# Kernel tuning notes

Hardware: AMD Instinct MI355X
Metric: run time of the kernel (lower is better)

## Reference

```python
import jax, jax.numpy as jnp
import numpy as np

N, E, G, H = 50000, 800000, 64, 4
IN_DIM, HID, OUT = 768, 256, 128
EPS = 1e-5
SLOPE = 0.2


def _glorot(k, shape):
    lim = np.sqrt(6.0 / (shape[0] + shape[1])).astype(np.float32)
    return jax.random.uniform(k, shape, jnp.float32, -lim, lim)


def setup_inputs() -> dict:
    key = jax.random.key(0)
    ks = jax.random.split(key, 24)
    inp = {
        'x': jax.random.normal(ks[0], (N, IN_DIM), jnp.float32),
        'edge_index': jax.random.randint(ks[1], (2, E), 0, N, jnp.int32),
        'batch': jnp.sort(jax.random.randint(ks[2], (N,), 0, G, jnp.int32)),
    }
    dims = [(IN_DIM, HID), (HID, HID), (HID, OUT)]
    for i, (di, do) in enumerate(dims, start=1):
        c = do // H
        inp[f'W{i}'] = _glorot(ks[3 * i], (di, do))
        inp[f'asrc{i}'] = _glorot(ks[3 * i + 1], (H, c))
        inp[f'adst{i}'] = _glorot(ks[3 * i + 2], (H, c))
        inp[f'b{i}'] = jnp.zeros((do,), jnp.float32)
        inp[f'g{i}'] = jnp.ones((do,), jnp.float32)
        inp[f'be{i}'] = jnp.zeros((do,), jnp.float32)
    return inp


def gat_conv(x, src, dst, W, asrc, adst, b):
    # PyG GATConv, concat=True, negative_slope=0.2, self-loops pre-appended.
    n = x.shape[0]
    HC = W.shape[1]
    C = HC // H
    h = (x @ W).reshape(n, H, C)                 # [N,H,C]
    e_src = (h * asrc).sum(-1)                   # [N,H]
    e_dst = (h * adst).sum(-1)                   # [N,H]
    e = jax.nn.leaky_relu(e_src[src] + e_dst[dst], SLOPE)  # [E',H]
    m = jax.ops.segment_max(e, dst, num_segments=n)
    p = jnp.exp(e - m[dst])
    denom = jax.ops.segment_sum(p, dst, num_segments=n)
    alpha = p / denom[dst]                       # segment softmax over in-edges
    out = jax.ops.segment_sum(alpha[:, :, None] * h[src], dst, num_segments=n)
    return out.reshape(n, HC) + b


def layer_norm(x, g, b):
    mu = x.mean(-1, keepdims=True)
    var = x.var(-1, keepdims=True)
    return g * (x - mu) * jax.lax.rsqrt(var + EPS) + b


def reference(x, edge_index, batch, W1, asrc1, adst1, b1, g1, be1,
              W2, asrc2, adst2, b2, g2, be2, W3, asrc3, adst3, b3, g3, be3):
    n = x.shape[0]
    loops = jnp.arange(n, dtype=edge_index.dtype)
    src = jnp.concatenate([edge_index[0], loops])
    dst = jnp.concatenate([edge_index[1], loops])
    h = gat_conv(x, src, dst, W1, asrc1, adst1, b1)
    h = layer_norm(jax.nn.elu(h), g1, be1)
    h = gat_conv(h, src, dst, W2, asrc2, adst2, b2)
    h = layer_norm(jax.nn.elu(h), g2, be2)
    h = gat_conv(h, src, dst, W3, asrc3, adst3, b3)
    node_emb = layer_norm(h, g3, be3)
    s = jax.ops.segment_sum(node_emb, batch, num_segments=G)
    cnt = jax.ops.segment_sum(jnp.ones((n, 1), node_emb.dtype), batch, num_segments=G)
    graph_emb = s / jnp.maximum(cnt, 1.0)
    return (node_emb, graph_emb)
```

## Files before the change

kernel.cpp:

```cpp
#include <hip/hip_runtime.h>
#include <math.h>

__device__ __forceinline__ float lrelu(float v) { return v > 0.f ? v : 0.2f * v; }
__device__ __forceinline__ float bf2f(ushort u) {
    return __uint_as_float(((unsigned int)u) << 16);
}
__device__ __forceinline__ ushort f2bf(float f) {
    unsigned int x = __float_as_uint(f);
    return (ushort)((x + 0x7fffu + ((x >> 16) & 1u)) >> 16);
}
__device__ __forceinline__ float wave_allred_sum(float v) {
#pragma unroll
    for (int off = 1; off < 64; off <<= 1) v += __shfl_xor(v, off, 64);
    return v;
}

typedef short bf16x8 __attribute__((ext_vector_type(8)));
typedef float f32x4 __attribute__((ext_vector_type(4)));

__global__ void hist_kernel(const int* __restrict__ dstrow, int* __restrict__ cnt,
                            int Etot, int E) {
    int i = blockIdx.x * blockDim.x + threadIdx.x;
    if (i >= Etot) return;
    int d = (i < E) ? dstrow[i] : (i - E);
    atomicAdd(&cnt[d], 1);
}

__global__ __launch_bounds__(256) void scan1_kernel(const int* __restrict__ cnt,
                                                    int* __restrict__ out,
                                                    int* __restrict__ btot, int n) {
    __shared__ int s[256];
    int i = blockIdx.x * 256 + threadIdx.x;
    int v = (i < n) ? cnt[i] : 0;
    s[threadIdx.x] = v;
    __syncthreads();
    for (int off = 1; off < 256; off <<= 1) {
        int t = (threadIdx.x >= off) ? s[threadIdx.x - off] : 0;
        __syncthreads();
        s[threadIdx.x] += t;
        __syncthreads();
    }
    if (i < n) out[i] = s[threadIdx.x];
    if (threadIdx.x == 255) btot[blockIdx.x] = s[255];
}
__global__ __launch_bounds__(1024) void scan2_kernel(int* __restrict__ btot, int nb) {
    __shared__ int s[1024];
    int tid = threadIdx.x;
    int v = (tid < nb) ? btot[tid] : 0;
    s[tid] = v;
    __syncthreads();
    for (int off = 1; off < 1024; off <<= 1) {
        int t = (tid >= off) ? s[tid - off] : 0;
        __syncthreads();
        s[tid] += t;
        __syncthreads();
    }
    if (tid < nb) btot[tid] = s[tid] - v;
}
__global__ void scan3_kernel(const int* __restrict__ scanned, const int* __restrict__ btot,
                             int* __restrict__ rowptr, int n) {
    int i = blockIdx.x * 256 + threadIdx.x;
    if (i < n) rowptr[i + 1] = scanned[i] + btot[i >> 8];
    if (i == 0) rowptr[0] = 0;
}

__global__ void fill_kernel(const int* __restrict__ srcrow, const int* __restrict__ dstrow,
                            const int* __restrict__ rowptr, int* __restrict__ pos,
                            int* __restrict__ srcs, int Etot, int E) {
    int i = blockIdx.x * blockDim.x + threadIdx.x;
    if (i >= Etot) return;
    int d = (i < E) ? dstrow[i] : (i - E);
    int s = (i < E) ? srcrow[i] : (i - E);
    int p = atomicAdd(&pos[d], 1);
    srcs[rowptr[d] + p] = s;
}

template <typename TA>
__global__ __launch_bounds__(256) void gemm_mfma(const TA* __restrict__ A,
                                                 const float* __restrict__ B,
                                                 ushort* __restrict__ C, int M, int K, int N) {
    __shared__ ushort As[128][40];
    __shared__ ushort Bs[128][40];
    int tid = threadIdx.x;
    int wave = tid >> 6, lane = tid & 63;
    int m0 = blockIdx.y * 128, n0 = blockIdx.x * 128;

    f32x4 acc[2][8] = {};

    int arow = tid >> 1;
    int ak = (tid & 1) * 16;
    int bk = tid >> 3;
    int bn = (tid & 7) * 16;

    int quad = lane >> 4;
    int mrow = lane & 15;

    for (int kt = 0; kt < K; kt += 32) {
        if (m0 + arow < M) {
            if constexpr (sizeof(TA) == 4) {
                const float* p = (const float*)A + (size_t)(m0 + arow) * K + kt + ak;
#pragma unroll
                for (int q = 0; q < 4; q++) {
                    float4 v = *(const float4*)(p + q * 4);
                    ushort* d = &As[arow][ak + q * 4];
                    d[0] = f2bf(v.x); d[1] = f2bf(v.y); d[2] = f2bf(v.z); d[3] = f2bf(v.w);
                }
            } else {
                const ushort* p = (const ushort*)A + (size_t)(m0 + arow) * K + kt + ak;
                *(uint4*)&As[arow][ak] = *(const uint4*)p;
                *(uint4*)&As[arow][ak + 8] = *(const uint4*)(p + 8);
            }
        } else {
#pragma unroll
            for (int q = 0; q < 16; q++) As[arow][ak + q] = 0;
        }
        {
            const float* p = B + (size_t)(kt + bk) * N + n0 + bn;
#pragma unroll
            for (int q = 0; q < 4; q++) {
                float4 v = *(const float4*)(p + q * 4);
                Bs[bn + q * 4 + 0][bk] = f2bf(v.x);
                Bs[bn + q * 4 + 1][bk] = f2bf(v.y);
                Bs[bn + q * 4 + 2][bk] = f2bf(v.z);
                Bs[bn + q * 4 + 3][bk] = f2bf(v.w);
            }
        }
        __syncthreads();
        bf16x8 afrag[2], bfrag[8];
#pragma unroll
        for (int r = 0; r < 2; r++)
            afrag[r] = *(const bf16x8*)&As[wave * 32 + r * 16 + mrow][quad * 8];
#pragma unroll
        for (int c = 0; c < 8; c++)
            bfrag[c] = *(const bf16x8*)&Bs[c * 16 + mrow][quad * 8];
#pragma unroll
        for (int r = 0; r < 2; r++)
#pragma unroll
            for (int c = 0; c < 8; c++)
                acc[r][c] = __builtin_amdgcn_mfma_f32_16x16x32_bf16(afrag[r], bfrag[c],
                                                                    acc[r][c], 0, 0, 0);
        __syncthreads();
    }
    int col = lane & 15;
#pragma unroll
    for (int r = 0; r < 2; r++) {
#pragma unroll
        for (int c = 0; c < 8; c++) {
#pragma unroll
            for (int reg = 0; reg < 4; reg++) {
                int gm = m0 + wave * 32 + r * 16 + quad * 4 + reg;
                int gn = n0 + c * 16 + col;
                if (gm < M) C[(size_t)gm * N + gn] = f2bf(acc[r][c][reg]);
            }
        }
    }
}

template <int VPL>
__global__ __launch_bounds__(256) void attn_wave(const ushort* __restrict__ H,
                                                 const float* __restrict__ asrc,
                                                 const float* __restrict__ adst,
                                                 float* __restrict__ es, float* __restrict__ ed,
                                                 int N) {
    constexpr int HC = VPL * 64;
    int lane = threadIdx.x & 63;
    int node = (blockIdx.x * blockDim.x + threadIdx.x) >> 6;
    if (node >= N) return;
    const ushort* hp = H + (size_t)node * HC + lane * VPL;
    float esum = 0.f, dsum = 0.f;
#pragma unroll
    for (int j = 0; j < VPL; j++) {
        float h = bf2f(hp[j]);
        int ch = lane * VPL + j;
        esum += h * asrc[ch];
        dsum += h * adst[ch];
    }
#pragma unroll
    for (int off = 1; off < 16; off <<= 1) {
        esum += __shfl_xor(esum, off, 64);
        dsum += __shfl_xor(dsum, off, 64);
    }
    if ((lane & 15) == 0) {
        int hh = lane >> 4;
        es[node * 4 + hh] = esum;
        ed[node * 4 + hh] = dsum;
    }
}

template <int VPL>
__global__ __launch_bounds__(256) void agg_gather(
    const ushort* __restrict__ H, const float* __restrict__ es, const float* __restrict__ ed,
    const int* __restrict__ rowptr, const int* __restrict__ srcs,
    const float* __restrict__ bias, const float* __restrict__ gamma,
    const float* __restrict__ beta, ushort* __restrict__ XoutB, float* __restrict__ XoutF,
    int N, int applyElu) {
    constexpr int HC = VPL * 64;
    int lane = threadIdx.x & 63;
    int node = (blockIdx.x * blockDim.x + threadIdx.x) >> 6;
    if (node >= N) return;
    int base = rowptr[node];
    int deg = rowptr[node + 1] - base;
    float4 ed4 = *(const float4*)&ed[node * 4];

    float4 sm = make_float4(0.f, 0.f, 0.f, 0.f);
    for (int i = lane; i < deg; i += 64) {
        int s = srcs[base + i];
        float4 e4 = *(const float4*)&es[(size_t)s * 4];
        sm.x += __expf(lrelu(e4.x + ed4.x));
        sm.y += __expf(lrelu(e4.y + ed4.y));
        sm.z += __expf(lrelu(e4.z + ed4.z));
        sm.w += __expf(lrelu(e4.w + ed4.w));
    }
    sm.x = wave_allred_sum(sm.x); sm.y = wave_allred_sum(sm.y);
    sm.z = wave_allred_sum(sm.z); sm.w = wave_allred_sum(sm.w);

    int hh = lane >> 4;
    float rd_h = 1.f / ((hh == 0) ? sm.x : (hh == 1) ? sm.y : (hh == 2) ? sm.z : sm.w);
    float edh = (hh == 0) ? ed4.x : (hh == 1) ? ed4.y : (hh == 2) ? ed4.z : ed4.w;

    float acc[VPL];
#pragma unroll
    for (int j = 0; j < VPL; j++) acc[j] = 0.f;
    const ushort* Hl = H + lane * VPL;

    int i = 0;
    for (; i + 2 <= deg; i += 2) {
        int s0 = srcs[base + i];
        int s1 = srcs[base + i + 1];
        float e0 = es[(size_t)s0 * 4 + hh];
        float e1 = es[(size_t)s1 * 4 + hh];
        const ushort* hp0 = Hl + (size_t)s0 * HC;
        const ushort* hp1 = Hl + (size_t)s1 * HC;
        float a0 = __expf(lrelu(e0 + edh)) * rd_h;
        float a1 = __expf(lrelu(e1 + edh)) * rd_h;
        if constexpr (VPL == 4) {
            ushort4 h0 = *(const ushort4*)hp0;
            ushort4 h1 = *(const ushort4*)hp1;
            acc[0] += a0 * bf2f(h0.x) + a1 * bf2f(h1.x);
            acc[1] += a0 * bf2f(h0.y) + a1 * bf2f(h1.y);
            acc[2] += a0 * bf2f(h0.z) + a1 * bf2f(h1.z);
            acc[3] += a0 * bf2f(h0.w) + a1 * bf2f(h1.w);
        } else {
            ushort2 h0 = *(const ushort2*)hp0;
            ushort2 h1 = *(const ushort2*)hp1;
            acc[0] += a0 * bf2f(h0.x) + a1 * bf2f(h1.x);
            acc[1] += a0 * bf2f(h0.y) + a1 * bf2f(h1.y);
        }
    }
    for (; i < deg; i++) {
        int s = srcs[base + i];
        float a = __expf(lrelu(es[(size_t)s * 4 + hh] + edh)) * rd_h;
        const ushort* hp = Hl + (size_t)s * HC;
        if constexpr (VPL == 4) {
            ushort4 hv = *(const ushort4*)hp;
            acc[0] += a * bf2f(hv.x); acc[1] += a * bf2f(hv.y);
            acc[2] += a * bf2f(hv.z); acc[3] += a * bf2f(hv.w);
        } else {
            ushort2 hv = *(const ushort2*)hp;
            acc[0] += a * bf2f(hv.x); acc[1] += a * bf2f(hv.y);
        }
    }

    float v[VPL];
    float s1 = 0.f, s2 = 0.f;
#pragma unroll
    for (int j = 0; j < VPL; j++) {
        int ch = lane * VPL + j;
        float t = acc[j] + bias[ch];
        if (applyElu) t = (t > 0.f) ? t : (__expf(t) - 1.f);
        v[j] = t;
        s1 += t;
        s2 += t * t;
    }
    s1 = wave_allred_sum(s1);
    s2 = wave_allred_sum(s2);
    float mu = s1 / (float)HC;
    float var = s2 / (float)HC - mu * mu;
    float rs = rsqrtf(var + 1e-5f);
#pragma unroll
    for (int j = 0; j < VPL; j++) {
        int ch = lane * VPL + j;
        float o = gamma[ch] * (v[j] - mu) * rs + beta[ch];
        if (XoutF) XoutF[(size_t)node * HC + ch] = o;
        else XoutB[(size_t)node * HC + ch] = f2bf(o);
    }
}

__global__ __launch_bounds__(128) void gsum_kernel(const float* __restrict__ node_emb,
                                                   const int* __restrict__ batch,
                                                   float* __restrict__ gsum,
                                                   int* __restrict__ gcnt, int N) {
    int start = blockIdx.x * 256;
    if (start >= N) return;
    int end = min(start + 256, N);
    int ch = threadIdx.x;
    float acc = 0.f;
    int runlen = 0;
    int curg = batch[start];
    for (int n = start; n < end; n++) {
        int g = batch[n];
        if (g != curg) {
            atomicAdd(&gsum[curg * 128 + ch], acc);
            if (ch == 0) atomicAdd(&gcnt[curg], runlen);
            acc = 0.f; runlen = 0; curg = g;
        }
        acc += node_emb[(size_t)n * 128 + ch];
        runlen++;
    }
    atomicAdd(&gsum[curg * 128 + ch], acc);
    if (ch == 0) atomicAdd(&gcnt[curg], runlen);
}

__global__ void gfinal_kernel(const float* __restrict__ gsum, const int* __restrict__ gcnt,
                              float* __restrict__ out, int Gn) {
    int i = blockIdx.x * blockDim.x + threadIdx.x;
    if (i >= Gn * 128) return;
    int g = i >> 7;
    out[i] = gsum[i] / fmaxf((float)gcnt[g], 1.f);
}

extern "C" void kernel_launch(void* const* d_in, const int* in_sizes, int n_in, void* d_out,
                              int out_size, void* d_ws, size_t ws_size, hipStream_t stream) {
    const float* x = (const float*)d_in[0];
    const int* ei = (const int*)d_in[1];
    const int* batch = (const int*)d_in[2];
    const float* W1 = (const float*)d_in[3];
    const float* as1 = (const float*)d_in[4];
    const float* ad1 = (const float*)d_in[5];
    const float* b1 = (const float*)d_in[6];
    const float* g1 = (const float*)d_in[7];
    const float* be1 = (const float*)d_in[8];
    const float* W2 = (const float*)d_in[9];
    const float* as2 = (const float*)d_in[10];
    const float* ad2 = (const float*)d_in[11];
    const float* b2 = (const float*)d_in[12];
    const float* g2 = (const float*)d_in[13];
    const float* be2 = (const float*)d_in[14];
    const float* W3 = (const float*)d_in[15];
    const float* as3 = (const float*)d_in[16];
    const float* ad3 = (const float*)d_in[17];
    const float* b3 = (const float*)d_in[18];
    const float* g3 = (const float*)d_in[19];
    const float* be3 = (const float*)d_in[20];

    int N = in_sizes[2];
    int E = in_sizes[1] / 2;
    int Etot = E + N;

    char* w = (char*)d_ws;
    size_t off = 0;
    auto alloc = [&](size_t bytes) -> void* {
        void* p = w + off;
        off += (bytes + 255) & ~(size_t)255;
        return p;
    };
    int* cnt = (int*)alloc((size_t)N * 4);
    int* pos = (int*)alloc((size_t)N * 4);
    float* gsum = (float*)alloc(64 * 128 * 4);
    int* gcnt = (int*)alloc(64 * 4);
    size_t zbytes = off;
    int* scantmp = (int*)alloc((size_t)N * 4);
    int* btot = (int*)alloc(1024 * 4);
    int* rowptr = (int*)alloc((size_t)(N + 1) * 4);
    int* srcs = (int*)alloc((size_t)Etot * 4);
    float* es = (float*)alloc((size_t)N * 16);
    float* ed = (float*)alloc((size_t)N * 16);
    ushort* Hb = (ushort*)alloc((size_t)N * 256 * 2);
    ushort* Xb = (ushort*)alloc((size_t)N * 256 * 2);

    hipMemsetAsync(d_ws, 0, zbytes, stream);

    const int* srcrow = ei;
    const int* dstrow = ei + E;

    int eb = (Etot + 255) / 256;
    int nb = (N + 255) / 256;
    hist_kernel<<<eb, 256, 0, stream>>>(dstrow, cnt, Etot, E);
    scan1_kernel<<<nb, 256, 0, stream>>>(cnt, scantmp, btot, N);
    scan2_kernel<<<1, 1024, 0, stream>>>(btot, nb);
    scan3_kernel<<<nb, 256, 0, stream>>>(scantmp, btot, rowptr, N);
    fill_kernel<<<eb, 256, 0, stream>>>(srcrow, dstrow, rowptr, pos, srcs, Etot, E);

    int mT = (N + 127) / 128;
    int nodeWaveBlocks = (N + 3) / 4;

    float* out_node = (float*)d_out;
    float* out_graph = (float*)d_out + (size_t)N * 128;

    gemm_mfma<float><<<dim3(2, mT), 256, 0, stream>>>(x, W1, Hb, N, 768, 256);
    attn_wave<4><<<nodeWaveBlocks, 256, 0, stream>>>(Hb, as1, ad1, es, ed, N);
    agg_gather<4><<<nodeWaveBlocks, 256, 0, stream>>>(Hb, es, ed, rowptr, srcs, b1, g1, be1,
                                                      Xb, nullptr, N, 1);
    gemm_mfma<ushort><<<dim3(2, mT), 256, 0, stream>>>(Xb, W2, Hb, N, 256, 256);
    attn_wave<4><<<nodeWaveBlocks, 256, 0, stream>>>(Hb, as2, ad2, es, ed, N);
    agg_gather<4><<<nodeWaveBlocks, 256, 0, stream>>>(Hb, es, ed, rowptr, srcs, b2, g2, be2,
                                                      Xb, nullptr, N, 1);
    gemm_mfma<ushort><<<dim3(1, mT), 256, 0, stream>>>(Xb, W3, Hb, N, 256, 128);
    attn_wave<2><<<nodeWaveBlocks, 256, 0, stream>>>(Hb, as3, ad3, es, ed, N);
    agg_gather<2><<<nodeWaveBlocks, 256, 0, stream>>>(Hb, es, ed, rowptr, srcs, b3, g3, be3,
                                                      nullptr, out_node, N, 0);
    gsum_kernel<<<(N + 255) / 256, 128, 0, stream>>>(out_node, batch, gsum, gcnt, N);
    gfinal_kernel<<<(64 * 128 + 255) / 256, 256, 0, stream>>>(gsum, gcnt, out_graph, 64);
}
```

Measured before the change: 820.7 us.

## Rewrite GEMM with async global-to-LDS double buffering and pretransposed bf16 weights

Weights are pre-transposed and converted to bf16 once per call by a new transpose kernel. The GEMM now stages A and B tiles straight into LDS with global_load_lds, double-buffered so the next K-slice loads while MFMAs run. It also uses XOR-swizzled LDS layouts to avoid bank conflicts and remaps workgroups across XCDs. The fp32 A tile is converted to bf16 at fragment-read time, which doubles LDS use for layer 1 and adds three small launches.

```diff
diff --git a/kernel.cpp b/kernel.cpp
--- a/kernel.cpp
+++ b/kernel.cpp
@@ -17,6 +17,12 @@
 
 typedef short bf16x8 __attribute__((ext_vector_type(8)));
 typedef float f32x4 __attribute__((ext_vector_type(4)));
+
+typedef const __attribute__((address_space(1))) void* gas_ptr;
+typedef __attribute__((address_space(3))) void* las_ptr;
+__device__ __forceinline__ void gload_lds16(const void* g, void* l) {
+    __builtin_amdgcn_global_load_lds((gas_ptr)g, (las_ptr)l, 16, 0, 0);
+}
 
 __global__ void hist_kernel(const int* __restrict__ dstrow, int* __restrict__ cnt,
                             int Etot, int E) {
@@ -75,64 +81,115 @@
     srcs[rowptr[d] + p] = s;
 }
 
+__global__ __launch_bounds__(256) void wconv_kernel(const float* __restrict__ W,
+                                                    ushort* __restrict__ Wt, int K, int N) {
+    __shared__ float t[32][33];
+    int k0 = blockIdx.x * 32, n0 = blockIdx.y * 32;
+    int tx = threadIdx.x & 31, ty = threadIdx.x >> 5;
+#pragma unroll
+    for (int i = 0; i < 32; i += 8)
+        t[ty + i][tx] = W[(size_t)(k0 + ty + i) * N + n0 + tx];
+    __syncthreads();
+#pragma unroll
+    for (int i = 0; i < 32; i += 8)
+        Wt[(size_t)(n0 + ty + i) * K + k0 + tx] = f2bf(t[tx][ty + i]);
+}
+
 template <typename TA>
-__global__ __launch_bounds__(256) void gemm_mfma(const TA* __restrict__ A,
-                                                 const float* __restrict__ B,
-                                                 ushort* __restrict__ C, int M, int K, int N) {
-    __shared__ ushort As[128][40];
-    __shared__ ushort Bs[128][40];
+__global__ __launch_bounds__(256) void gemm_mfma2(const TA* __restrict__ A,
+                                                  const ushort* __restrict__ Wt,
+                                                  ushort* __restrict__ C,
+                                                  int M, int K, int N) {
+    constexpr bool F32A = (sizeof(TA) == 4);
+    constexpr int ASZ = F32A ? 16384 : 8192;
+    __shared__ __align__(16) unsigned char smem[2 * ASZ + 16384];
+
     int tid = threadIdx.x;
-    int wave = tid >> 6, lane = tid & 63;
-    int m0 = blockIdx.y * 128, n0 = blockIdx.x * 128;
+    int wv = tid >> 6, lane = tid & 63;
+    int quad = lane >> 4, mrow = lane & 15;
+
+    int nwg = gridDim.x * gridDim.y;
+    int id = blockIdx.y * gridDim.x + blockIdx.x;
+    int q8 = nwg >> 3, r8 = nwg & 7;
+    int xcd = id & 7, loc = id >> 3;
+    int wgid = (xcd < r8 ? xcd * (q8 + 1) : r8 * (q8 + 1) + (xcd - r8) * q8) + loc;
+    int n0 = (wgid % gridDim.x) * 128;
+    int m0 = (wgid / gridDim.x) * 128;
 
     f32x4 acc[2][8] = {};
 
-    int arow = tid >> 1;
-    int ak = (tid & 1) * 16;
-    int bk = tid >> 3;
-    int bn = (tid & 7) * 16;
-
-    int quad = lane >> 4;
-    int mrow = lane & 15;
-
-    for (int kt = 0; kt < K; kt += 32) {
-        if (m0 + arow < M) {
-            if constexpr (sizeof(TA) == 4) {
-                const float* p = (const float*)A + (size_t)(m0 + arow) * K + kt + ak;
-#pragma unroll
-                for (int q = 0; q < 4; q++) {
-                    float4 v = *(const float4*)(p + q * 4);
-                    ushort* d = &As[arow][ak + q * 4];
-                    d[0] = f2bf(v.x); d[1] = f2bf(v.y); d[2] = f2bf(v.z); d[3] = f2bf(v.w);
-                }
-            } else {
-                const ushort* p = (const ushort*)A + (size_t)(m0 + arow) * K + kt + ak;
-                *(uint4*)&As[arow][ak] = *(const uint4*)p;
-                *(uint4*)&As[arow][ak + 8] = *(const uint4*)(p + 8);
+    auto stageA = [&](int kt, int buf) {
+        unsigned char* lb = smem + buf * ASZ;
+        if constexpr (F32A) {
+#pragma unroll
+            for (int q = 0; q < 4; q++) {
+                int row = q * 32 + (tid >> 3);
+                int gch = (tid & 7) ^ (row & 7);
+                int rc = min(m0 + row, M - 1);
+                gload_lds16((const float*)A + (size_t)rc * K + kt + gch * 4,
+                            lb + q * 4096 + tid * 16);
             }
         } else {
 #pragma unroll
-            for (int q = 0; q < 16; q++) As[arow][ak + q] = 0;
-        }
-        {
-            const float* p = B + (size_t)(kt + bk) * N + n0 + bn;
-#pragma unroll
-            for (int q = 0; q < 4; q++) {
-                float4 v = *(const float4*)(p + q * 4);
-                Bs[bn + q * 4 + 0][bk] = f2bf(v.x);
-                Bs[bn + q * 4 + 1][bk] = f2bf(v.y);
-                Bs[bn + q * 4 + 2][bk] = f2bf(v.z);
-                Bs[bn + q * 4 + 3][bk] = f2bf(v.w);
+            for (int q = 0; q < 2; q++) {
+                int row = q * 64 + (tid >> 2);
+                int gch = (tid & 3) ^ ((row & 3) ^ ((row >> 2) & 1));
+                int rc = min(m0 + row, M - 1);
+                gload_lds16((const ushort*)A + (size_t)rc * K + kt + gch * 8,
+                            lb + q * 4096 + tid * 16);
             }
         }
-        __syncthreads();
+    };
+    auto stageB = [&](int kt, int buf) {
+        unsigned char* lb = smem + 2 * ASZ + buf * 8192;
+#pragma unroll
+        for (int q = 0; q < 2; q++) {
+            int row = q * 64 + (tid >> 2);
+            int gch = (tid & 3) ^ ((row & 3) ^ ((row >> 2) & 1));
+            gload_lds16(Wt + (size_t)(n0 + row) * K + kt + gch * 8,
+                        lb + q * 4096 + tid * 16);
+        }
+    };
+
+    int nsteps = K >> 5;
+    stageA(0, 0);
+    stageB(0, 0);
+    __syncthreads();
+
+    for (int s = 0; s < nsteps; s++) {
+        int kt = s << 5;
+        if (s + 1 < nsteps) {
+            stageA(kt + 32, (s + 1) & 1);
+            stageB(kt + 32, (s + 1) & 1);
+        }
+        const unsigned char* la = smem + (s & 1) * ASZ;
+        const unsigned char* lbB = smem + 2 * ASZ + (s & 1) * 8192;
+
         bf16x8 afrag[2], bfrag[8];
 #pragma unroll
-        for (int r = 0; r < 2; r++)
-            afrag[r] = *(const bf16x8*)&As[wave * 32 + r * 16 + mrow][quad * 8];
-#pragma unroll
-        for (int c = 0; c < 8; c++)
-            bfrag[c] = *(const bf16x8*)&Bs[c * 16 + mrow][quad * 8];
+        for (int r = 0; r < 2; r++) {
+            int row = wv * 32 + r * 16 + mrow;
+            if constexpr (F32A) {
+                int f = row & 7;
+                float4 x0 = *(const float4*)(la + row * 128 + ((quad * 2 + 0) ^ f) * 16);
+                float4 x1 = *(const float4*)(la + row * 128 + ((quad * 2 + 1) ^ f) * 16);
+                union { bf16x8 v; ushort u[8]; } t;
+                t.u[0] = f2bf(x0.x); t.u[1] = f2bf(x0.y);
+                t.u[2] = f2bf(x0.z); t.u[3] = f2bf(x0.w);
+                t.u[4] = f2bf(x1.x); t.u[5] = f2bf(x1.y);
+                t.u[6] = f2bf(x1.z); t.u[7] = f2bf(x1.w);
+                afrag[r] = t.v;
+            } else {
+                int f = (row & 3) ^ ((row >> 2) & 1);
+                afrag[r] = *(const bf16x8*)(la + row * 64 + (quad ^ f) * 16);
+            }
+        }
+#pragma unroll
+        for (int c = 0; c < 8; c++) {
+            int row = c * 16 + mrow;
+            int f = (row & 3) ^ ((row >> 2) & 1);
+            bfrag[c] = *(const bf16x8*)(lbB + row * 64 + (quad ^ f) * 16);
+        }
 #pragma unroll
         for (int r = 0; r < 2; r++)
 #pragma unroll
@@ -141,6 +198,7 @@
                                                                     acc[r][c], 0, 0, 0);
         __syncthreads();
     }
+
     int col = lane & 15;
 #pragma unroll
     for (int r = 0; r < 2; r++) {
@@ -148,7 +206,7 @@
         for (int c = 0; c < 8; c++) {
 #pragma unroll
             for (int reg = 0; reg < 4; reg++) {
-                int gm = m0 + wave * 32 + r * 16 + quad * 4 + reg;
+                int gm = m0 + wv * 32 + r * 16 + quad * 4 + reg;
                 int gn = n0 + c * 16 + col;
                 if (gm < M) C[(size_t)gm * N + gn] = f2bf(acc[r][c][reg]);
             }
@@ -367,11 +425,18 @@
     float* ed = (float*)alloc((size_t)N * 16);
     ushort* Hb = (ushort*)alloc((size_t)N * 256 * 2);
     ushort* Xb = (ushort*)alloc((size_t)N * 256 * 2);
+    ushort* wt1 = (ushort*)alloc((size_t)768 * 256 * 2);
+    ushort* wt2 = (ushort*)alloc((size_t)256 * 256 * 2);
+    ushort* wt3 = (ushort*)alloc((size_t)256 * 128 * 2);
 
     hipMemsetAsync(d_ws, 0, zbytes, stream);
 
     const int* srcrow = ei;
     const int* dstrow = ei + E;
+
+    wconv_kernel<<<dim3(768 / 32, 256 / 32), 256, 0, stream>>>(W1, wt1, 768, 256);
+    wconv_kernel<<<dim3(256 / 32, 256 / 32), 256, 0, stream>>>(W2, wt2, 256, 256);
+    wconv_kernel<<<dim3(256 / 32, 128 / 32), 256, 0, stream>>>(W3, wt3, 256, 128);
 
     int eb = (Etot + 255) / 256;
     int nb = (N + 255) / 256;
@@ -387,15 +452,15 @@
     float* out_node = (float*)d_out;
     float* out_graph = (float*)d_out + (size_t)N * 128;
 
-    gemm_mfma<float><<<dim3(2, mT), 256, 0, stream>>>(x, W1, Hb, N, 768, 256);
+    gemm_mfma2<float><<<dim3(2, mT), 256, 0, stream>>>(x, wt1, Hb, N, 768, 256);
     attn_wave<4><<<nodeWaveBlocks, 256, 0, stream>>>(Hb, as1, ad1, es, ed, N);
     agg_gather<4><<<nodeWaveBlocks, 256, 0, stream>>>(Hb, es, ed, rowptr, srcs, b1, g1, be1,
                                                       Xb, nullptr, N, 1);
-    gemm_mfma<ushort><<<dim3(2, mT), 256, 0, stream>>>(Xb, W2, Hb, N, 256, 256);
+    gemm_mfma2<ushort><<<dim3(2, mT), 256, 0, stream>>>(Xb, wt2, Hb, N, 256, 256);
     attn_wave<4><<<nodeWaveBlocks, 256, 0, stream>>>(Hb, as2, ad2, es, ed, N);
     agg_gather<4><<<nodeWaveBlocks, 256, 0, stream>>>(Hb, es, ed, rowptr, srcs, b2, g2, be2,
                                                       Xb, nullptr, N, 1);
-    gemm_mfma<ushort><<<dim3(1, mT), 256, 0, stream>>>(Xb, W3, Hb, N, 256, 128);
+    gemm_mfma2<ushort><<<dim3(1, mT), 256, 0, stream>>>(Xb, wt3, Hb, N, 256, 128);
     attn_wave<2><<<nodeWaveBlocks, 256, 0, stream>>>(Hb, as3, ad3, es, ed, N);
     agg_gather<2><<<nodeWaveBlocks, 256, 0, stream>>>(Hb, es, ed, rowptr, srcs, b3, g3, be3,
                                                       nullptr, out_node, N, 0);
```

Result: faster. 770.9 us (-6.1%).
